# Kernel optimization log

Hardware: AMD Instinct MI355X
Metric: run time of the kernel (lower is better)

## Reference

```python
import jax, jax.numpy as jnp
import numpy as np

D_MODEL = 1024
D_STATE = 64
D_CONV = 4
HEADDIM = 64
EXPAND = 2
NGROUPS = 1
D_INNER = EXPAND * D_MODEL            # 2048
NHEADS = D_INNER // HEADDIM           # 32
CONV_DIM = D_INNER + 2 * NGROUPS * D_STATE
D_IN_PROJ = 2 * D_INNER + 2 * NGROUPS * D_STATE + NHEADS
FFN_DIM = 4096
B_SZ = 2
SEQ = 2048


def layernorm(x, w, b, eps=1e-5):
    m = jnp.mean(x, axis=-1, keepdims=True)
    v = jnp.var(x, axis=-1, keepdims=True)
    return (x - m) * jax.lax.rsqrt(v + eps) * w + b


def silu(x):
    return x * jax.nn.sigmoid(x)


def causal_dwconv(x, w, b):
    # x: [B, L, C], w: [C, K] depthwise, b: [C]; causal (left) padding
    xc = jnp.transpose(x, (0, 2, 1))                       # [B, C, L]
    xc = jnp.pad(xc, ((0, 0), (0, 0), (D_CONV - 1, 0)))
    k = w[:, None, :]                                      # [C, 1, K]
    y = jax.lax.conv_general_dilated(
        xc, k, window_strides=(1,), padding='VALID',
        dimension_numbers=('NCH', 'OIH', 'NCH'),
        feature_group_count=CONV_DIM)
    return jnp.transpose(y, (0, 2, 1)) + b                 # [B, L, C]


def mamba2(x, in_proj_w, conv_w, conv_b, dt_bias, A_log, D_param, norm_w, out_proj_w):
    Bsz, L, _ = x.shape
    zxbcdt = x @ in_proj_w.T                               # [B, L, D_IN_PROJ]
    z, xBC, dt = jnp.split(zxbcdt, [D_INNER, D_INNER + CONV_DIM], axis=-1)
    dt = jax.nn.softplus(dt + dt_bias)                     # [B, L, H]
    xBC = silu(causal_dwconv(xBC, conv_w, conv_b))
    xs, Bm, Cm = jnp.split(xBC, [D_INNER, D_INNER + NGROUPS * D_STATE], axis=-1)
    xs = xs.reshape(Bsz, L, NHEADS, HEADDIM)
    Bm = Bm.reshape(Bsz, L, NGROUPS, D_STATE)
    Cm = Cm.reshape(Bsz, L, NGROUPS, D_STATE)
    hpg = NHEADS // NGROUPS
    Bh = jnp.repeat(Bm, hpg, axis=2)                       # [B, L, H, N]
    Ch = jnp.repeat(Cm, hpg, axis=2)                       # [B, L, H, N]
    A = -jnp.exp(A_log)                                    # [H]
    dA = jnp.exp(dt * A)                                   # [B, L, H]

    # time-major for scan
    def step(h, inp):
        dA_t, dt_t, x_t, B_t, C_t = inp                    # [B,H], [B,H], [B,H,P], [B,H,N], [B,H,N]
        h = h * dA_t[:, :, None, None] + (dt_t[:, :, None, None] * x_t[..., None]) * B_t[:, :, None, :]
        y_t = jnp.einsum('bhpn,bhn->bhp', h, C_t)
        return h, y_t

    h0 = jnp.zeros((Bsz, NHEADS, HEADDIM, D_STATE), dtype=x.dtype)
    xs_tm = (jnp.moveaxis(dA, 1, 0), jnp.moveaxis(dt, 1, 0),
             jnp.moveaxis(xs, 1, 0), jnp.moveaxis(Bh, 1, 0), jnp.moveaxis(Ch, 1, 0))
    _, ys = jax.lax.scan(step, h0, xs_tm)                  # [L, B, H, P]
    y = jnp.moveaxis(ys, 0, 1) + D_param[None, None, :, None] * xs
    y = y.reshape(Bsz, L, D_INNER)
    # gated RMSNorm: RMSNorm(y * silu(z)) * weight
    y = y * silu(z)
    y = y * jax.lax.rsqrt(jnp.mean(jnp.square(y), axis=-1, keepdims=True) + 1e-5) * norm_w
    return y @ out_proj_w.T                                # [B, L, D_MODEL]


def setup_inputs() -> dict:
    key = jax.random.key(0)
    ks = jax.random.split(key, 12)
    s = 0.02
    inp = {
        'x': jax.random.normal(ks[0], (B_SZ, SEQ, D_MODEL), dtype=jnp.float32),
        'ln0_w': jnp.ones((D_MODEL,), jnp.float32), 'ln0_b': jnp.zeros((D_MODEL,), jnp.float32),
        'ln1_w': jnp.ones((D_MODEL,), jnp.float32), 'ln1_b': jnp.zeros((D_MODEL,), jnp.float32),
        'ln2_w': jnp.ones((D_MODEL,), jnp.float32), 'ln2_b': jnp.zeros((D_MODEL,), jnp.float32),
        'in_proj_w': jax.random.normal(ks[1], (D_IN_PROJ, D_MODEL), jnp.float32) * s,
        'conv_w': jax.random.normal(ks[2], (CONV_DIM, D_CONV), jnp.float32) * 0.2,
        'conv_b': jnp.zeros((CONV_DIM,), jnp.float32),
        'dt_bias': jax.random.uniform(ks[3], (NHEADS,), jnp.float32, -4.0, -1.0),
        'A_log': jnp.log(jnp.arange(1, NHEADS + 1, dtype=jnp.float32)),
        'D_param': jnp.ones((NHEADS,), jnp.float32),
        'norm_w': jnp.ones((D_INNER,), jnp.float32),
        'out_proj_w': jax.random.normal(ks[4], (D_MODEL, D_INNER), jnp.float32) * s,
        'ffn_w1': jax.random.normal(ks[5], (FFN_DIM, D_MODEL), jnp.float32) * s,
        'ffn_b1': jnp.zeros((FFN_DIM,), jnp.float32),
        'ffn_w2': jax.random.normal(ks[6], (D_MODEL, FFN_DIM), jnp.float32) * s,
        'ffn_b2': jnp.zeros((D_MODEL,), jnp.float32),
    }
    return inp


def reference(x, ln0_w, ln0_b, ln1_w, ln1_b, ln2_w, ln2_b, in_proj_w, conv_w, conv_b,
              dt_bias, A_log, D_param, norm_w, out_proj_w, ffn_w1, ffn_b1, ffn_w2, ffn_b2):
    x = layernorm(x, ln0_w, ln0_b)                                  # ln0 (layer_id==0)
    m = mamba2(layernorm(x, ln1_w, ln1_b), in_proj_w, conv_w, conv_b,
               dt_bias, A_log, D_param, norm_w, out_proj_w)
    x = x + m                                                        # dropout is identity in eval
    h = layernorm(x, ln2_w, ln2_b)
    h = jax.nn.gelu(h @ ffn_w1.T + ffn_b1, approximate=False) @ ffn_w2.T + ffn_b2
    return x + h
```

## Files before the change

kernel.cpp:

```cpp
#include <hip/hip_runtime.h>
#include <hip/hip_bf16.h>
#include <math.h>

typedef __hip_bfloat16 bf16;
typedef __bf16 bhalf;
typedef bhalf bhalf8 __attribute__((ext_vector_type(8)));
typedef float f32x4 __attribute__((ext_vector_type(4)));
typedef unsigned short u16;
typedef u16 u16x4 __attribute__((ext_vector_type(4)));

#define D_MODEL   1024
#define D_STATE   64
#define HEADDIM   64
#define D_INNER   2048
#define NHEADS    32
#define CONV_DIM  2176
#define D_IN_PROJ 4256
#define FFN_DIM   4096
#define BSZ       2
#define SEQ       2048
#define NROWS     (BSZ*SEQ)
#define TC        64
#define NCH       (SEQ/TC)

#define AS1 __attribute__((address_space(1)))
#define AS3 __attribute__((address_space(3)))
__device__ __forceinline__ void load_lds16(const void* g, void* l) {
  __builtin_amdgcn_global_load_lds((AS1 void*)g, (AS3 void*)l, 16, 0, 0);
}

__global__ __launch_bounds__(64)
void detect_kernel(const unsigned short* __restrict__ x, int* __restrict__ flagp)
{
  int bad = 0;
  for (int i = threadIdx.x; i < 4096; i += 64) {
    unsigned u = ((unsigned)x[i]) << 16;
    float v = __uint_as_float(u);
    if (!(fabsf(v) <= 1e6f)) bad = 1;
  }
  unsigned long long any = __ballot(bad);
  if (threadIdx.x == 0) *flagp = (any != 0ULL) ? 1 : 0;
}

#define NT 19
struct CvtArgs {
  const void* src[NT];
  void*       dst[NT];
  int ccum[NT + 1];
  int nel[NT];
};

__global__ __launch_bounds__(256)
void cvt_kernel(CvtArgs a, const int* __restrict__ flagp)
{
  int c = blockIdx.x;
  int ti = 0;
  while (c >= a.ccum[ti + 1]) ti++;
  int base = (c - a.ccum[ti]) * 2048;
  int n = a.nel[ti];
  if (*flagp) {
    const float* s = (const float*)a.src[ti];
    bf16* d = (bf16*)a.dst[ti];
    for (int i = threadIdx.x; i < 2048; i += 256) {
      int j = base + i;
      if (j < n) d[j] = __float2bfloat16(s[j]);
    }
  } else {
    const unsigned short* s = (const unsigned short*)a.src[ti];
    unsigned short* d = (unsigned short*)a.dst[ti];
    for (int i = threadIdx.x; i < 2048; i += 256) {
      int j = base + i;
      if (j < n) d[j] = s[j];
    }
  }
}

template<int EPI>
__global__ __launch_bounds__(256, 2)
void gemm_bt(const bf16* __restrict__ A, const bf16* __restrict__ W,
             int M, int N, int K,
             bf16* __restrict__ outB,
             const bf16* __restrict__ bias)
{
  __shared__ __align__(16) bhalf sA[128 * 64];
  __shared__ __align__(16) bhalf sW[128 * 64];
  const int t    = threadIdx.x;
  const int n0   = blockIdx.x * 128;
  const int m0   = blockIdx.y * 128;
  const int w    = t >> 6;
  const int lane = t & 63;
  const int wm   = (w >> 1) * 64;
  const int wn   = (w & 1) * 64;
  const int lr   = lane & 15;
  const int lq   = lane >> 4;

  f32x4 acc[4][4];
  #pragma unroll
  for (int i = 0; i < 4; i++)
    #pragma unroll
    for (int j = 0; j < 4; j++)
      acc[i][j] = (f32x4){0.f, 0.f, 0.f, 0.f};

  for (int k0 = 0; k0 < K; k0 += 64) {
    #pragma unroll
    for (int j = 0; j < 4; j++) {
      int s  = t + 256 * j;
      int r  = s >> 3;
      int cs = (s & 7) ^ (r & 7);
      load_lds16(A + (size_t)(m0 + r) * K + k0 + cs * 8, sA + s * 8);
      int wr = n0 + r; wr = wr < N ? wr : N - 1;
      load_lds16(W + (size_t)wr * K + k0 + cs * 8, sW + s * 8);
    }
    __syncthreads();
    #pragma unroll
    for (int kk = 0; kk < 2; kk++) {
      bhalf8 af[4], bfr[4];
      #pragma unroll
      for (int i = 0; i < 4; i++) {
        int r = wm + i * 16 + lr;
        int c = (kk * 4 + lq) ^ (r & 7);
        af[i] = *(const bhalf8*)(sA + r * 64 + c * 8);
      }
      #pragma unroll
      for (int j = 0; j < 4; j++) {
        int r = wn + j * 16 + lr;
        int c = (kk * 4 + lq) ^ (r & 7);
        bfr[j] = *(const bhalf8*)(sW + r * 64 + c * 8);
      }
      #pragma unroll
      for (int i = 0; i < 4; i++)
        #pragma unroll
        for (int j = 0; j < 4; j++)
          acc[i][j] = __builtin_amdgcn_mfma_f32_16x16x32_bf16(af[i], bfr[j], acc[i][j], 0, 0, 0);
    }
    __syncthreads();
  }

  #pragma unroll
  for (int i = 0; i < 4; i++) {
    #pragma unroll
    for (int j = 0; j < 4; j++) {
      #pragma unroll
      for (int r = 0; r < 4; r++) {
        int m = m0 + wm + i * 16 + lq * 4 + r;
        int n = n0 + wn + j * 16 + lr;
        if (n < N) {
          float v = acc[i][j][r];
          size_t idx = (size_t)m * N + n;
          if (EPI == 0) {
            outB[idx] = __float2bfloat16(v);
          } else {
            v += __bfloat162float(bias[n]);
            outB[idx] = __float2bfloat16(0.5f * v * (1.0f + erff(v * 0.70710678118654752f)));
          }
        }
      }
    }
  }
}

struct SkParts { float* p0; float* p1; float* p2; float* p3; };

__global__ __launch_bounds__(256, 2)
void gemm_sk(const bf16* __restrict__ A, const bf16* __restrict__ W,
             int M, int N, int K, int ks, SkParts parts)
{
  __shared__ __align__(16) bhalf sA[128 * 64];
  __shared__ __align__(16) bhalf sW[128 * 64];
  const int t    = threadIdx.x;
  const int n0   = blockIdx.x * 128;
  const int m0   = blockIdx.y * 128;
  const int z    = blockIdx.z;
  const int w    = t >> 6;
  const int lane = t & 63;
  const int wm   = (w >> 1) * 64;
  const int wn   = (w & 1) * 64;
  const int lr   = lane & 15;
  const int lq   = lane >> 4;

  f32x4 acc[4][4];
  #pragma unroll
  for (int i = 0; i < 4; i++)
    #pragma unroll
    for (int j = 0; j < 4; j++)
      acc[i][j] = (f32x4){0.f, 0.f, 0.f, 0.f};

  const int kend = z * ks + ks;
  for (int k0 = z * ks; k0 < kend; k0 += 64) {
    #pragma unroll
    for (int j = 0; j < 4; j++) {
      int s  = t + 256 * j;
      int r  = s >> 3;
      int cs = (s & 7) ^ (r & 7);
      load_lds16(A + (size_t)(m0 + r) * K + k0 + cs * 8, sA + s * 8);
      load_lds16(W + (size_t)(n0 + r) * K + k0 + cs * 8, sW + s * 8);
    }
    __syncthreads();
    #pragma unroll
    for (int kk = 0; kk < 2; kk++) {
      bhalf8 af[4], bfr[4];
      #pragma unroll
      for (int i = 0; i < 4; i++) {
        int r = wm + i * 16 + lr;
        int c = (kk * 4 + lq) ^ (r & 7);
        af[i] = *(const bhalf8*)(sA + r * 64 + c * 8);
      }
      #pragma unroll
      for (int j = 0; j < 4; j++) {
        int r = wn + j * 16 + lr;
        int c = (kk * 4 + lq) ^ (r & 7);
        bfr[j] = *(const bhalf8*)(sW + r * 64 + c * 8);
      }
      #pragma unroll
      for (int i = 0; i < 4; i++)
        #pragma unroll
        for (int j = 0; j < 4; j++)
          acc[i][j] = __builtin_amdgcn_mfma_f32_16x16x32_bf16(af[i], bfr[j], acc[i][j], 0, 0, 0);
    }
    __syncthreads();
  }

  float* out = (z == 0) ? parts.p0 : (z == 1) ? parts.p1 : (z == 2) ? parts.p2 : parts.p3;
  #pragma unroll
  for (int i = 0; i < 4; i++)
    #pragma unroll
    for (int j = 0; j < 4; j++)
      #pragma unroll
      for (int r = 0; r < 4; r++) {
        int m = m0 + wm + i * 16 + lq * 4 + r;
        int n = n0 + wn + j * 16 + lr;
        out[(size_t)m * N + n] = acc[i][j][r];
      }
}

__global__ __launch_bounds__(256)
void reduce_out_kernel(const float* __restrict__ p0, const float* __restrict__ p1,
                       const bf16* __restrict__ resB, float* __restrict__ out)
{
  int i = blockIdx.x * 256 + threadIdx.x;
  f32x4 a = ((const f32x4*)p0)[i];
  f32x4 b = ((const f32x4*)p1)[i];
  u16x4 r = ((const u16x4*)resB)[i];
  f32x4 o;
  #pragma unroll
  for (int j = 0; j < 4; j++)
    o[j] = a[j] + b[j] + __uint_as_float(((unsigned)r[j]) << 16);
  ((f32x4*)out)[i] = o;
}

__global__ __launch_bounds__(256)
void reduce_ffn_kernel(const float* __restrict__ p0, const float* __restrict__ p1,
                       const float* __restrict__ p2, const float* __restrict__ p3,
                       const bf16* __restrict__ bias, const float* __restrict__ resF,
                       void* __restrict__ outp, const int* __restrict__ flagp)
{
  int i = blockIdx.x * 256 + threadIdx.x;
  int n4 = i & (D_MODEL / 4 - 1);
  f32x4 v0 = ((const f32x4*)p0)[i];
  f32x4 v1 = ((const f32x4*)p1)[i];
  f32x4 v2 = ((const f32x4*)p2)[i];
  f32x4 v3 = ((const f32x4*)p3)[i];
  f32x4 rf = ((const f32x4*)resF)[i];
  u16x4 bb = ((const u16x4*)bias)[n4];
  f32x4 o;
  #pragma unroll
  for (int j = 0; j < 4; j++)
    o[j] = ((v0[j] + v1[j]) + (v2[j] + v3[j])) + rf[j] +
           __uint_as_float(((unsigned)bb[j]) << 16);
  if (*flagp) {
    ((f32x4*)outp)[i] = o;
  } else {
    bf16* ob = (bf16*)outp;
    #pragma unroll
    for (int j = 0; j < 4; j++) ob[i * 4 + j] = __float2bfloat16(o[j]);
  }
}

__global__ __launch_bounds__(256)
void ln01_kernel(const bf16* __restrict__ x,
                 const bf16* __restrict__ w0, const bf16* __restrict__ b0,
                 const bf16* __restrict__ w1, const bf16* __restrict__ b1,
                 bf16* __restrict__ x0o, bf16* __restrict__ x1o)
{
  int row = blockIdx.x, t = threadIdx.x;
  const bf16* xr = x + (size_t)row * D_MODEL;
  __shared__ float rs[4], rq[4];
  float v[4], s = 0.f, ss = 0.f;
  #pragma unroll
  for (int i = 0; i < 4; i++) {
    v[i] = __bfloat162float(xr[t + 256 * i]);
    s += v[i]; ss += v[i] * v[i];
  }
  #pragma unroll
  for (int o = 32; o; o >>= 1) { s += __shfl_down(s, o); ss += __shfl_down(ss, o); }
  if ((t & 63) == 0) { rs[t >> 6] = s; rq[t >> 6] = ss; }
  __syncthreads();
  float S = rs[0] + rs[1] + rs[2] + rs[3];
  float Q = rq[0] + rq[1] + rq[2] + rq[3];
  float mean = S * (1.f / D_MODEL);
  float rstd = rsqrtf(Q * (1.f / D_MODEL) - mean * mean + 1e-5f);
  float u[4]; s = 0.f; ss = 0.f;
  #pragma unroll
  for (int i = 0; i < 4; i++) {
    int c = t + 256 * i;
    u[i] = (v[i] - mean) * rstd * __bfloat162float(w0[c]) + __bfloat162float(b0[c]);
    s += u[i]; ss += u[i] * u[i];
    x0o[(size_t)row * D_MODEL + c] = __float2bfloat16(u[i]);
  }
  __syncthreads();
  #pragma unroll
  for (int o = 32; o; o >>= 1) { s += __shfl_down(s, o); ss += __shfl_down(ss, o); }
  if ((t & 63) == 0) { rs[t >> 6] = s; rq[t >> 6] = ss; }
  __syncthreads();
  S = rs[0] + rs[1] + rs[2] + rs[3];
  Q = rq[0] + rq[1] + rq[2] + rq[3];
  mean = S * (1.f / D_MODEL);
  rstd = rsqrtf(Q * (1.f / D_MODEL) - mean * mean + 1e-5f);
  #pragma unroll
  for (int i = 0; i < 4; i++) {
    int c = t + 256 * i;
    x1o[(size_t)row * D_MODEL + c] =
        __float2bfloat16((u[i] - mean) * rstd * __bfloat162float(w1[c]) + __bfloat162float(b1[c]));
  }
}

__global__ __launch_bounds__(256)
void conv_silu_kernel(const bf16* __restrict__ zxb, const bf16* __restrict__ cw,
                      const bf16* __restrict__ cb, bf16* __restrict__ xact)
{
  int c = blockIdx.x * 256 + threadIdx.x;
  int row = blockIdx.y;
  if (c >= CONV_DIM) return;
  int l = row & (SEQ - 1);
  float acc = __bfloat162float(cb[c]);
  #pragma unroll
  for (int k = 0; k < 4; k++) {
    int lt = l - 3 + k;
    if (lt >= 0)
      acc += __bfloat162float(zxb[(size_t)(row - 3 + k) * D_IN_PROJ + D_INNER + c]) *
             __bfloat162float(cw[c * 4 + k]);
  }
  xact[(size_t)row * CONV_DIM + c] = __float2bfloat16(acc / (1.f + expf(-acc)));
}

__global__ __launch_bounds__(256)
void dt_kernel(const bf16* __restrict__ zxb, const bf16* __restrict__ dt_bias,
               const bf16* __restrict__ A_log, float* __restrict__ dts,
               float* __restrict__ ldab)
{
  int i = blockIdx.x * 256 + threadIdx.x;
  int row = i >> 5, h = i & 31;
  float v = __bfloat162float(zxb[(size_t)row * D_IN_PROJ + (D_INNER + CONV_DIM) + h]) +
            __bfloat162float(dt_bias[h]);
  float sp = (v > 20.f) ? v : log1pf(expf(v));
  dts[i] = sp;
  ldab[i] = -sp * expf(__bfloat162float(A_log[h]));
}

__global__ __launch_bounds__(256)
void scan_state_kernel(const bf16* __restrict__ xact, const float* __restrict__ dts,
                       const float* __restrict__ ldab, bf16* __restrict__ Sbuf,
                       float* __restrict__ acb)
{
  __shared__ __align__(16) bf16 wBT[64][72];
  __shared__ __align__(16) bf16 XT[64][72];
  __shared__ float lsS[64], dtS[64];
  const int bid = blockIdx.x;
  const int bh = bid & 63, c = bid >> 6;
  const int b = bh >> 5, h = bh & 31;
  const int t0 = c * TC;
  const int tid = threadIdx.x;
  const int w = tid >> 6, lane = tid & 63;
  const int lr = lane & 15, lq = lane >> 4;

  if (w == 0) {
    float v = ldab[(size_t)(b * SEQ + t0 + lane) * NHEADS + h];
    #pragma unroll
    for (int o = 1; o < 64; o <<= 1) {
      float up = __shfl_up(v, o);
      if (lane >= o) v += up;
    }
    lsS[lane] = v;
    dtS[lane] = dts[(size_t)(b * SEQ + t0 + lane) * NHEADS + h];
  }
  __syncthreads();
  const float lsT = lsS[63];
  {
    int nn = tid & 63, u0 = (tid >> 6) * 16;
    for (int i = 0; i < 16; i++) {
      int u = u0 + i;
      const bf16* rowp = xact + (size_t)(b * SEQ + t0 + u) * CONV_DIM;
      float wgt = dtS[u] * __expf(lsT - lsS[u]);
      wBT[nn][u] = __float2bfloat16(__bfloat162float(rowp[D_INNER + nn]) * wgt);
      XT[nn][u]  = rowp[h * 64 + nn];
    }
  }
  __syncthreads();

  bhalf8 af0 = *(const bhalf8*)&wBT[16 * w + lr][lq * 8];
  bhalf8 af1 = *(const bhalf8*)&wBT[16 * w + lr][32 + lq * 8];
  bf16* sb = Sbuf + ((size_t)bh * NCH + c) * 4096;
  #pragma unroll
  for (int jt = 0; jt < 4; jt++) {
    bhalf8 xf0 = *(const bhalf8*)&XT[16 * jt + lr][lq * 8];
    bhalf8 xf1 = *(const bhalf8*)&XT[16 * jt + lr][32 + lq * 8];
    f32x4 acc = (f32x4){0.f, 0.f, 0.f, 0.f};
    acc = __builtin_amdgcn_mfma_f32_16x16x32_bf16(af0, xf0, acc, 0, 0, 0);
    acc = __builtin_amdgcn_mfma_f32_16x16x32_bf16(af1, xf1, acc, 0, 0, 0);
    #pragma unroll
    for (int r = 0; r < 4; r++) {
      int n = 16 * w + lq * 4 + r;
      int p = 16 * jt + lr;
      sb[p * 64 + n] = __float2bfloat16(acc[r]);
    }
  }
  if (tid == 0) acb[bh * NCH + c] = __expf(lsT);
}

__global__ __launch_bounds__(256)
void state_prop_kernel(bf16* __restrict__ Sbuf, const float* __restrict__ acb)
{
  const int bh = blockIdx.x >> 2, q = blockIdx.x & 3;
  const int t = threadIdx.x;
  bf16* sp = Sbuf + (size_t)bh * NCH * 4096 + q * 1024 + t;
  const float* ap = acb + bh * NCH;
  float h0 = 0.f, h1 = 0.f, h2 = 0.f, h3 = 0.f;
  for (int c = 0; c < NCH; c++) {
    bf16* pc = sp + (size_t)c * 4096;
    float s0 = __bfloat162float(pc[0]);
    float s1 = __bfloat162float(pc[256]);
    float s2 = __bfloat162float(pc[512]);
    float s3 = __bfloat162float(pc[768]);
    float a = ap[c];
    pc[0]   = __float2bfloat16(h0);
    pc[256] = __float2bfloat16(h1);
    pc[512] = __float2bfloat16(h2);
    pc[768] = __float2bfloat16(h3);
    h0 = fmaf(h0, a, s0); h1 = fmaf(h1, a, s1);
    h2 = fmaf(h2, a, s2); h3 = fmaf(h3, a, s3);
  }
}

__global__ __launch_bounds__(256)
void scan_y_kernel(const bf16* __restrict__ xact, const float* __restrict__ dts,
                   const float* __restrict__ ldab, const bf16* __restrict__ Sbuf,
                   bf16* __restrict__ yfull)
{
  __shared__ __align__(16) bf16 Cs[64][72];
  __shared__ __align__(16) bf16 Bs[64][72];
  __shared__ __align__(16) bf16 XT[64][72];
  __shared__ __align__(16) bf16 HT[64][72];
  __shared__ __align__(16) bf16 Ms[64][72];
  __shared__ float lsS[64], dtS[64];
  const int bid = blockIdx.x;
  const int bh = bid & 63, c = bid >> 6;
  const int b = bh >> 5, h = bh & 31;
  const int t0 = c * TC;
  const int tid = threadIdx.x;
  const int w = tid >> 6, lane = tid & 63;
  const int lr = lane & 15, lq = lane >> 4;

  if (w == 0) {
    float v = ldab[(size_t)(b * SEQ + t0 + lane) * NHEADS + h];
    #pragma unroll
    for (int o = 1; o < 64; o <<= 1) {
      float up = __shfl_up(v, o);
      if (lane >= o) v += up;
    }
    lsS[lane] = v;
    dtS[lane] = dts[(size_t)(b * SEQ + t0 + lane) * NHEADS + h];
  }
  {
    int nn = tid & 63, u0 = (tid >> 6) * 16;
    for (int i = 0; i < 16; i++) {
      int u = u0 + i;
      const bf16* rowp = xact + (size_t)(b * SEQ + t0 + u) * CONV_DIM;
      Bs[u][nn] = rowp[D_INNER + nn];
      Cs[u][nn] = rowp[D_INNER + 64 + nn];
      XT[nn][u] = rowp[h * 64 + nn];
    }
    const bf16* sb = Sbuf + ((size_t)bh * NCH + c) * 4096;
    for (int i = 0; i < 16; i++) {
      int e = tid + 256 * i;
      HT[e >> 6][e & 63] = sb[e];
    }
  }
  __syncthreads();

  bhalf8 cf0 = *(const bhalf8*)&Cs[16 * w + lr][lq * 8];
  bhalf8 cf1 = *(const bhalf8*)&Cs[16 * w + lr][32 + lq * 8];
  f32x4 accH[4];
  #pragma unroll
  for (int jt = 0; jt < 4; jt++) {
    bhalf8 bf0 = *(const bhalf8*)&Bs[16 * jt + lr][lq * 8];
    bhalf8 bf1 = *(const bhalf8*)&Bs[16 * jt + lr][32 + lq * 8];
    f32x4 g = (f32x4){0.f, 0.f, 0.f, 0.f};
    g = __builtin_amdgcn_mfma_f32_16x16x32_bf16(cf0, bf0, g, 0, 0, 0);
    g = __builtin_amdgcn_mfma_f32_16x16x32_bf16(cf1, bf1, g, 0, 0, 0);
    bhalf8 hf0 = *(const bhalf8*)&HT[16 * jt + lr][lq * 8];
    bhalf8 hf1 = *(const bhalf8*)&HT[16 * jt + lr][32 + lq * 8];
    f32x4 ah = (f32x4){0.f, 0.f, 0.f, 0.f};
    ah = __builtin_amdgcn_mfma_f32_16x16x32_bf16(cf0, hf0, ah, 0, 0, 0);
    ah = __builtin_amdgcn_mfma_f32_16x16x32_bf16(cf1, hf1, ah, 0, 0, 0);
    accH[jt] = ah;
    #pragma unroll
    for (int r = 0; r < 4; r++) {
      int t = 16 * w + lq * 4 + r;
      int u = 16 * jt + lr;
      float m = 0.f;
      if (u <= t) m = g[r] * __expf(lsS[t] - lsS[u]) * dtS[u];
      Ms[t][u] = __float2bfloat16(m);
    }
  }
  __syncthreads();

  bhalf8 mf0 = *(const bhalf8*)&Ms[16 * w + lr][lq * 8];
  bhalf8 mf1 = *(const bhalf8*)&Ms[16 * w + lr][32 + lq * 8];
  #pragma unroll
  for (int jt = 0; jt < 4; jt++) {
    bhalf8 xf0 = *(const bhalf8*)&XT[16 * jt + lr][lq * 8];
    bhalf8 xf1 = *(const bhalf8*)&XT[16 * jt + lr][32 + lq * 8];
    f32x4 acc = (f32x4){0.f, 0.f, 0.f, 0.f};
    acc = __builtin_amdgcn_mfma_f32_16x16x32_bf16(mf0, xf0, acc, 0, 0, 0);
    acc = __builtin_amdgcn_mfma_f32_16x16x32_bf16(mf1, xf1, acc, 0, 0, 0);
    #pragma unroll
    for (int r = 0; r < 4; r++) {
      int t = 16 * w + lq * 4 + r;
      int p = 16 * jt + lr;
      float y = acc[r] + __expf(lsS[t]) * accH[jt][r];
      yfull[(size_t)(b * SEQ + t0 + t) * D_INNER + h * 64 + p] = __float2bfloat16(y);
    }
  }
}

__global__ __launch_bounds__(256)
void gate_rms_kernel(const bf16* __restrict__ yfull, const bf16* __restrict__ xact,
                     const bf16* __restrict__ zxb, const bf16* __restrict__ Dp,
                     const bf16* __restrict__ nw, bf16* __restrict__ yn)
{
  int row = blockIdx.x, t = threadIdx.x;
  __shared__ float rq[4];
  float yv[8]; float ss = 0.f;
  #pragma unroll
  for (int i = 0; i < 8; i++) {
    int c = t + 256 * i;
    float y = __bfloat162float(yfull[(size_t)row * D_INNER + c]) +
              __bfloat162float(Dp[c >> 6]) *
              __bfloat162float(xact[(size_t)row * CONV_DIM + c]);
    float z = __bfloat162float(zxb[(size_t)row * D_IN_PROJ + c]);
    yv[i] = y * (z / (1.f + expf(-z)));
    ss += yv[i] * yv[i];
  }
  #pragma unroll
  for (int o = 32; o; o >>= 1) ss += __shfl_down(ss, o);
  if ((t & 63) == 0) rq[t >> 6] = ss;
  __syncthreads();
  float tot = rq[0] + rq[1] + rq[2] + rq[3];
  float rr = rsqrtf(tot * (1.f / D_INNER) + 1e-5f);
  #pragma unroll
  for (int i = 0; i < 8; i++) {
    int c = t + 256 * i;
    yn[(size_t)row * D_INNER + c] =
        __float2bfloat16(yv[i] * rr * __bfloat162float(nw[c]));
  }
}

__global__ __launch_bounds__(256)
void ln2_kernel(const float* __restrict__ xin, const bf16* __restrict__ w,
                const bf16* __restrict__ b, bf16* __restrict__ out)
{
  int row = blockIdx.x, t = threadIdx.x;
  const float* xr = xin + (size_t)row * D_MODEL;
  __shared__ float rs[4], rq[4];
  float v[4], s = 0.f, ss = 0.f;
  #pragma unroll
  for (int i = 0; i < 4; i++) {
    v[i] = xr[t + 256 * i];
    s += v[i]; ss += v[i] * v[i];
  }
  #pragma unroll
  for (int o = 32; o; o >>= 1) { s += __shfl_down(s, o); ss += __shfl_down(ss, o); }
  if ((t & 63) == 0) { rs[t >> 6] = s; rq[t >> 6] = ss; }
  __syncthreads();
  float S = rs[0] + rs[1] + rs[2] + rs[3];
  float Q = rq[0] + rq[1] + rq[2] + rq[3];
  float mean = S * (1.f / D_MODEL);
  float rstd = rsqrtf(Q * (1.f / D_MODEL) - mean * mean + 1e-5f);
  #pragma unroll
  for (int i = 0; i < 4; i++) {
    int c = t + 256 * i;
    out[(size_t)row * D_MODEL + c] =
        __float2bfloat16((v[i] - mean) * rstd * __bfloat162float(w[c]) + __bfloat162float(b[c]));
  }
}

extern "C" void kernel_launch(void* const* d_in, const int* in_sizes, int n_in,
                              void* d_out, int out_size, void* d_ws, size_t ws_size,
                              hipStream_t stream)
{
  char* ws = (char*)d_ws;
  bf16*  xcvt  = (bf16*) (ws + 0);
  bf16*  x1b   = (bf16*) (ws + 8388608);
  bf16*  Sbuf  = (bf16*) (ws + 0);
  bf16*  ynb   = (bf16*) (ws + 0);
  float* pf0   = (float*)(ws + 0);
  bf16*  wproj = (bf16*) (ws + 16777216);
  float* acb   = (float*)(ws + 16777216);
  float* dtsb  = (float*)(ws + 16785408);
  float* ldab  = (float*)(ws + 17309696);
  float* pf1   = (float*)(ws + 16777216);
  bf16*  wout  = (bf16*) (ws + 25493504);
  bf16*  w1c   = (bf16*) (ws + 29687808);
  bf16*  w2c   = (bf16*) (ws + 38076416);
  bf16*  ln0w  = (bf16*) (ws + 46465024);
  bf16*  ln0b  = (bf16*) (ws + 46467072);
  bf16*  ln1w  = (bf16*) (ws + 46469120);
  bf16*  ln1b  = (bf16*) (ws + 46471168);
  bf16*  ln2w  = (bf16*) (ws + 46473216);
  bf16*  ln2b  = (bf16*) (ws + 46475264);
  bf16*  convw = (bf16*) (ws + 46477312);
  bf16*  convb = (bf16*) (ws + 46494720);
  bf16*  dtb   = (bf16*) (ws + 46499072);
  bf16*  alog  = (bf16*) (ws + 46499136);
  bf16*  Dp    = (bf16*) (ws + 46499200);
  bf16*  normw = (bf16*) (ws + 46499264);
  bf16*  b1c   = (bf16*) (ws + 46503360);
  bf16*  b2c   = (bf16*) (ws + 46511552);
  int*   flag  = (int*)  (ws + 46513600);
  bf16*  x0b   = (bf16*) (ws + 46514176);
  bf16*  zxb   = (bf16*) (ws + 54902784);
  float* x2f   = (float*)(ws + 54902784);
  float* pf3   = (float*)(ws + 71680000);
  bf16*  xact  = (bf16*) (ws + 89767936);
  float* pout0 = (float*)(ws + 89767936);
  float* pout1 = (float*)(ws + 106545152);
  bf16*  gbuf  = (bf16*) (ws + 89767936);
  bf16*  yfull = (bf16*) (ws + 125419520);
  bf16*  hln   = (bf16*) (ws + 125419520);
  float* pf2   = (float*)(ws + 125419520);

  detect_kernel<<<1, 64, 0, stream>>>((const unsigned short*)d_in[0], flag);

  CvtArgs ca;
  void* dsts[NT] = { xcvt, ln0w, ln0b, ln1w, ln1b, ln2w, ln2b, wproj, convw, convb,
                     dtb, alog, Dp, normw, wout, w1c, b1c, w2c, b2c };
  int cc = 0;
  ca.ccum[0] = 0;
  for (int i = 0; i < NT; i++) {
    ca.src[i] = d_in[i];
    ca.dst[i] = dsts[i];
    ca.nel[i] = in_sizes[i];
    cc += (in_sizes[i] + 2047) / 2048;
    ca.ccum[i + 1] = cc;
  }
  cvt_kernel<<<cc, 256, 0, stream>>>(ca, flag);

  ln01_kernel<<<NROWS, 256, 0, stream>>>(xcvt, ln0w, ln0b, ln1w, ln1b, x0b, x1b);

  gemm_bt<0><<<dim3(34, 32), 256, 0, stream>>>(x1b, wproj, NROWS, D_IN_PROJ, D_MODEL,
                                               zxb, nullptr);

  conv_silu_kernel<<<dim3(9, NROWS), 256, 0, stream>>>(zxb, convw, convb, xact);
  dt_kernel<<<(NROWS * NHEADS) / 256, 256, 0, stream>>>(zxb, dtb, alog, dtsb, ldab);

  scan_state_kernel<<<NCH * 64, 256, 0, stream>>>(xact, dtsb, ldab, Sbuf, acb);
  state_prop_kernel<<<64 * 4, 256, 0, stream>>>(Sbuf, acb);
  scan_y_kernel<<<NCH * 64, 256, 0, stream>>>(xact, dtsb, ldab, Sbuf, yfull);

  gate_rms_kernel<<<NROWS, 256, 0, stream>>>(yfull, xact, zxb, Dp, normw, ynb);

  SkParts po = { pout0, pout1, pout0, pout0 };
  gemm_sk<<<dim3(8, 32, 2), 256, 0, stream>>>(ynb, wout, NROWS, D_MODEL, D_INNER, 1024, po);
  reduce_out_kernel<<<(NROWS * D_MODEL) / 1024, 256, 0, stream>>>(pout0, pout1, x0b, x2f);

  ln2_kernel<<<NROWS, 256, 0, stream>>>(x2f, ln2w, ln2b, hln);

  gemm_bt<2><<<dim3(32, 32), 256, 0, stream>>>(hln, w1c, NROWS, FFN_DIM, D_MODEL,
                                               gbuf, b1c);

  SkParts pfp = { pf0, pf1, pf2, pf3 };
  gemm_sk<<<dim3(8, 32, 4), 256, 0, stream>>>(gbuf, w2c, NROWS, D_MODEL, FFN_DIM, 1024, pfp);
  reduce_ffn_kernel<<<(NROWS * D_MODEL) / 1024, 256, 0, stream>>>(pf0, pf1, pf2, pf3,
                                                                  b2c, x2f, d_out, flag);
}
```

Measured before the change: 481.0 us.

## Replace split-K GEMMs and reductions with 64-row tiles, fused epilogues, grouped block order

The out-proj and FFN2 GEMMs no longer use split-K with fp32 partial buffers and separate reduce kernels. A new 64x128-tile kernel runs over the full K and fuses the residual add, bias and output cast into its epilogue. Blocks in both GEMM kernels now use a 1D grid remapped into groups of 8 M-tiles, meant to improve L2 reuse of weight tiles. This removes the partial-sum traffic and two launches, but each block now walks a longer K loop with a smaller M tile, so there is less parallel split work.

```diff
diff --git a/kernel.cpp b/kernel.cpp
--- a/kernel.cpp
+++ b/kernel.cpp
@@ -78,15 +78,21 @@
 template<int EPI>
 __global__ __launch_bounds__(256, 2)
 void gemm_bt(const bf16* __restrict__ A, const bf16* __restrict__ W,
-             int M, int N, int K,
+             int M, int N, int K, int nb,
              bf16* __restrict__ outB,
              const bf16* __restrict__ bias)
 {
   __shared__ __align__(16) bhalf sA[128 * 64];
   __shared__ __align__(16) bhalf sW[128 * 64];
+  const int id   = blockIdx.x;
+  const int per  = nb * 8;
+  const int hi   = id / per;
+  const int rem  = id - hi * per;
+  const int jn   = rem >> 3;
+  const int mi   = hi * 8 + (rem & 7);
+  const int n0   = jn * 128;
+  const int m0   = mi * 128;
   const int t    = threadIdx.x;
-  const int n0   = blockIdx.x * 128;
-  const int m0   = blockIdx.y * 128;
   const int w    = t >> 6;
   const int lane = t & 63;
   const int wm   = (w >> 1) * 64;
@@ -159,48 +165,63 @@
   }
 }
 
-struct SkParts { float* p0; float* p1; float* p2; float* p3; };
-
+template<int EPI>
 __global__ __launch_bounds__(256, 2)
-void gemm_sk(const bf16* __restrict__ A, const bf16* __restrict__ W,
-             int M, int N, int K, int ks, SkParts parts)
-{
-  __shared__ __align__(16) bhalf sA[128 * 64];
+void gemm_skinny(const bf16* __restrict__ A, const bf16* __restrict__ W,
+                 int M, int N, int K,
+                 float* __restrict__ outF, void* __restrict__ outAny,
+                 const bf16* __restrict__ bias,
+                 const bf16* __restrict__ resB,
+                 const float* __restrict__ resF,
+                 const int* __restrict__ flagp)
+{
+  __shared__ __align__(16) bhalf sA[64 * 64];
   __shared__ __align__(16) bhalf sW[128 * 64];
+  const int id   = blockIdx.x;
+  const int hi   = id >> 6;
+  const int rem  = id & 63;
+  const int jn   = rem >> 3;
+  const int mi   = hi * 8 + (rem & 7);
+  const int m0   = mi * 64;
+  const int n0   = jn * 128;
   const int t    = threadIdx.x;
-  const int n0   = blockIdx.x * 128;
-  const int m0   = blockIdx.y * 128;
-  const int z    = blockIdx.z;
   const int w    = t >> 6;
   const int lane = t & 63;
-  const int wm   = (w >> 1) * 64;
+  const int wm   = (w >> 1) * 32;
   const int wn   = (w & 1) * 64;
   const int lr   = lane & 15;
   const int lq   = lane >> 4;
 
-  f32x4 acc[4][4];
-  #pragma unroll
-  for (int i = 0; i < 4; i++)
+  f32x4 acc[2][4];
+  #pragma unroll
+  for (int i = 0; i < 2; i++)
     #pragma unroll
     for (int j = 0; j < 4; j++)
       acc[i][j] = (f32x4){0.f, 0.f, 0.f, 0.f};
 
-  const int kend = z * ks + ks;
-  for (int k0 = z * ks; k0 < kend; k0 += 64) {
-    #pragma unroll
-    for (int j = 0; j < 4; j++) {
-      int s  = t + 256 * j;
-      int r  = s >> 3;
-      int cs = (s & 7) ^ (r & 7);
-      load_lds16(A + (size_t)(m0 + r) * K + k0 + cs * 8, sA + s * 8);
-      load_lds16(W + (size_t)(n0 + r) * K + k0 + cs * 8, sW + s * 8);
+  for (int k0 = 0; k0 < K; k0 += 64) {
+    {
+      #pragma unroll
+      for (int j = 0; j < 2; j++) {
+        int s  = t + 256 * j;
+        int r  = s >> 3;
+        int cs = (s & 7) ^ (r & 7);
+        load_lds16(A + (size_t)(m0 + r) * K + k0 + cs * 8, sA + s * 8);
+      }
+      #pragma unroll
+      for (int j = 0; j < 4; j++) {
+        int s  = t + 256 * j;
+        int r  = s >> 3;
+        int cs = (s & 7) ^ (r & 7);
+        load_lds16(W + (size_t)(n0 + r) * K + k0 + cs * 8, sW + s * 8);
+      }
     }
     __syncthreads();
     #pragma unroll
     for (int kk = 0; kk < 2; kk++) {
-      bhalf8 af[4], bfr[4];
-      #pragma unroll
-      for (int i = 0; i < 4; i++) {
+      bhalf8 af[2], bfr[4];
+      #pragma unroll
+      for (int i = 0; i < 2; i++) {
         int r = wm + i * 16 + lr;
         int c = (kk * 4 + lq) ^ (r & 7);
         af[i] = *(const bhalf8*)(sA + r * 64 + c * 8);
@@ -212,7 +233,7 @@
         bfr[j] = *(const bhalf8*)(sW + r * 64 + c * 8);
       }
       #pragma unroll
-      for (int i = 0; i < 4; i++)
+      for (int i = 0; i < 2; i++)
         #pragma unroll
         for (int j = 0; j < 4; j++)
           acc[i][j] = __builtin_amdgcn_mfma_f32_16x16x32_bf16(af[i], bfr[j], acc[i][j], 0, 0, 0);
@@ -220,59 +241,26 @@
     __syncthreads();
   }
 
-  float* out = (z == 0) ? parts.p0 : (z == 1) ? parts.p1 : (z == 2) ? parts.p2 : parts.p3;
-  #pragma unroll
-  for (int i = 0; i < 4; i++)
-    #pragma unroll
-    for (int j = 0; j < 4; j++)
+  const bool f32o = (EPI == 1) && (*flagp != 0);
+  #pragma unroll
+  for (int i = 0; i < 2; i++) {
+    #pragma unroll
+    for (int j = 0; j < 4; j++) {
       #pragma unroll
       for (int r = 0; r < 4; r++) {
         int m = m0 + wm + i * 16 + lq * 4 + r;
         int n = n0 + wn + j * 16 + lr;
-        out[(size_t)m * N + n] = acc[i][j][r];
-      }
-}
-
-__global__ __launch_bounds__(256)
-void reduce_out_kernel(const float* __restrict__ p0, const float* __restrict__ p1,
-                       const bf16* __restrict__ resB, float* __restrict__ out)
-{
-  int i = blockIdx.x * 256 + threadIdx.x;
-  f32x4 a = ((const f32x4*)p0)[i];
-  f32x4 b = ((const f32x4*)p1)[i];
-  u16x4 r = ((const u16x4*)resB)[i];
-  f32x4 o;
-  #pragma unroll
-  for (int j = 0; j < 4; j++)
-    o[j] = a[j] + b[j] + __uint_as_float(((unsigned)r[j]) << 16);
-  ((f32x4*)out)[i] = o;
-}
-
-__global__ __launch_bounds__(256)
-void reduce_ffn_kernel(const float* __restrict__ p0, const float* __restrict__ p1,
-                       const float* __restrict__ p2, const float* __restrict__ p3,
-                       const bf16* __restrict__ bias, const float* __restrict__ resF,
-                       void* __restrict__ outp, const int* __restrict__ flagp)
-{
-  int i = blockIdx.x * 256 + threadIdx.x;
-  int n4 = i & (D_MODEL / 4 - 1);
-  f32x4 v0 = ((const f32x4*)p0)[i];
-  f32x4 v1 = ((const f32x4*)p1)[i];
-  f32x4 v2 = ((const f32x4*)p2)[i];
-  f32x4 v3 = ((const f32x4*)p3)[i];
-  f32x4 rf = ((const f32x4*)resF)[i];
-  u16x4 bb = ((const u16x4*)bias)[n4];
-  f32x4 o;
-  #pragma unroll
-  for (int j = 0; j < 4; j++)
-    o[j] = ((v0[j] + v1[j]) + (v2[j] + v3[j])) + rf[j] +
-           __uint_as_float(((unsigned)bb[j]) << 16);
-  if (*flagp) {
-    ((f32x4*)outp)[i] = o;
-  } else {
-    bf16* ob = (bf16*)outp;
-    #pragma unroll
-    for (int j = 0; j < 4; j++) ob[i * 4 + j] = __float2bfloat16(o[j]);
+        size_t idx = (size_t)m * N + n;
+        float v = acc[i][j][r];
+        if (EPI == 0) {
+          outF[idx] = v + __bfloat162float(resB[idx]);
+        } else {
+          v += __bfloat162float(bias[n]) + resF[idx];
+          if (f32o) ((float*)outAny)[idx] = v;
+          else      ((bf16*)outAny)[idx] = __float2bfloat16(v);
+        }
+      }
+    }
   }
 }
 
@@ -603,12 +591,10 @@
   bf16*  x1b   = (bf16*) (ws + 8388608);
   bf16*  Sbuf  = (bf16*) (ws + 0);
   bf16*  ynb   = (bf16*) (ws + 0);
-  float* pf0   = (float*)(ws + 0);
   bf16*  wproj = (bf16*) (ws + 16777216);
   float* acb   = (float*)(ws + 16777216);
   float* dtsb  = (float*)(ws + 16785408);
   float* ldab  = (float*)(ws + 17309696);
-  float* pf1   = (float*)(ws + 16777216);
   bf16*  wout  = (bf16*) (ws + 25493504);
   bf16*  w1c   = (bf16*) (ws + 29687808);
   bf16*  w2c   = (bf16*) (ws + 38076416);
@@ -630,14 +616,10 @@
   bf16*  x0b   = (bf16*) (ws + 46514176);
   bf16*  zxb   = (bf16*) (ws + 54902784);
   float* x2f   = (float*)(ws + 54902784);
-  float* pf3   = (float*)(ws + 71680000);
   bf16*  xact  = (bf16*) (ws + 89767936);
-  float* pout0 = (float*)(ws + 89767936);
-  float* pout1 = (float*)(ws + 106545152);
   bf16*  gbuf  = (bf16*) (ws + 89767936);
   bf16*  yfull = (bf16*) (ws + 125419520);
   bf16*  hln   = (bf16*) (ws + 125419520);
-  float* pf2   = (float*)(ws + 125419520);
 
   detect_kernel<<<1, 64, 0, stream>>>((const unsigned short*)d_in[0], flag);
 
@@ -657,8 +639,8 @@
 
   ln01_kernel<<<NROWS, 256, 0, stream>>>(xcvt, ln0w, ln0b, ln1w, ln1b, x0b, x1b);
 
-  gemm_bt<0><<<dim3(34, 32), 256, 0, stream>>>(x1b, wproj, NROWS, D_IN_PROJ, D_MODEL,
-                                               zxb, nullptr);
+  gemm_bt<0><<<34 * 32, 256, 0, stream>>>(x1b, wproj, NROWS, D_IN_PROJ, D_MODEL, 34,
+                                          zxb, nullptr);
 
   conv_silu_kernel<<<dim3(9, NROWS), 256, 0, stream>>>(zxb, convw, convb, xact);
   dt_kernel<<<(NROWS * NHEADS) / 256, 256, 0, stream>>>(zxb, dtb, alog, dtsb, ldab);
@@ -669,17 +651,14 @@
 
   gate_rms_kernel<<<NROWS, 256, 0, stream>>>(yfull, xact, zxb, Dp, normw, ynb);
 
-  SkParts po = { pout0, pout1, pout0, pout0 };
-  gemm_sk<<<dim3(8, 32, 2), 256, 0, stream>>>(ynb, wout, NROWS, D_MODEL, D_INNER, 1024, po);
-  reduce_out_kernel<<<(NROWS * D_MODEL) / 1024, 256, 0, stream>>>(pout0, pout1, x0b, x2f);
+  gemm_skinny<0><<<512, 256, 0, stream>>>(ynb, wout, NROWS, D_MODEL, D_INNER,
+                                          x2f, nullptr, nullptr, x0b, nullptr, flag);
 
   ln2_kernel<<<NROWS, 256, 0, stream>>>(x2f, ln2w, ln2b, hln);
 
-  gemm_bt<2><<<dim3(32, 32), 256, 0, stream>>>(hln, w1c, NROWS, FFN_DIM, D_MODEL,
-                                               gbuf, b1c);
-
-  SkParts pfp = { pf0, pf1, pf2, pf3 };
-  gemm_sk<<<dim3(8, 32, 4), 256, 0, stream>>>(gbuf, w2c, NROWS, D_MODEL, FFN_DIM, 1024, pfp);
-  reduce_ffn_kernel<<<(NROWS * D_MODEL) / 1024, 256, 0, stream>>>(pf0, pf1, pf2, pf3,
-                                                                  b2c, x2f, d_out, flag);
-}
+  gemm_bt<2><<<32 * 32, 256, 0, stream>>>(hln, w1c, NROWS, FFN_DIM, D_MODEL, 32,
+                                          gbuf, b1c);
+
+  gemm_skinny<1><<<512, 256, 0, stream>>>(gbuf, w2c, NROWS, D_MODEL, FFN_DIM,
+                                          nullptr, d_out, b2c, nullptr, x2f, flag);
+}
```

Result: no change. 477.8 us (-0.7%).
